# Kernel tuning notes

Measured on AMD Instinct MI355X. Metric: run time of the kernel, lower is better.

## Reference

```python
import jax, jax.numpy as jnp
import numpy as np

NB_HEAD = 16
SIZE_PER_HEAD = 64
D_MODEL = NB_HEAD * SIZE_PER_HEAD  # 1024
B, S = 4, 2048
NEG_BIG = 1e10


def setup_inputs() -> dict:
    key = jax.random.key(0)
    ks = jax.random.split(key, 9)
    glorot = lambda k, shape: jax.random.uniform(
        k, shape, jnp.float32, -1.0, 1.0) * np.sqrt(6.0 / (shape[0] + shape[1]))
    return {
        "Q_emb": jax.random.normal(ks[0], (B, S, D_MODEL), jnp.float32),
        "K_emb": jax.random.normal(ks[1], (B, S, D_MODEL), jnp.float32),
        "V_emb": jax.random.normal(ks[2], (B, S, D_MODEL), jnp.float32),
        "Q_ini": jax.random.randint(ks[3], (B, S), 0, 50),
        "K_ini": jax.random.randint(ks[4], (B, S), 0, 50),
        "WQ": glorot(ks[5], (D_MODEL, D_MODEL)),
        "WK": glorot(ks[6], (D_MODEL, D_MODEL)),
        "WV": glorot(ks[7], (D_MODEL, D_MODEL)),
        "WO": glorot(ks[8], (D_MODEL, D_MODEL)),
    }


def _proj(x, W):
    # [B,S,D] @ [D, H*dh] -> [B,H,S,dh]
    b, s, _ = x.shape
    y = jnp.einsum('bsd,de->bse', x, W)
    return y.reshape(b, s, NB_HEAD, SIZE_PER_HEAD).transpose(0, 2, 1, 3)


def reference(Q_emb, K_emb, V_emb, Q_ini, K_ini, WQ, WK, WV, WO):
    b, sq, _ = Q_emb.shape
    sk = K_emb.shape[1]
    q = _proj(Q_emb, WQ)
    k = _proj(K_emb, WK)
    v = _proj(V_emb, WV)
    scores = jnp.einsum('bhqd,bhkd->bhqk', q, k) / jnp.sqrt(
        jnp.asarray(SIZE_PER_HEAD, scores_dtype := q.dtype))
    # pad mask: 1 where key token id != 0, broadcast over queries
    pad = (K_ini != 0).astype(scores.dtype)[:, None, None, :]  # [B,1,1,Sk]
    # sub mask: cumsum of eye along rows == lower-triangular causal mask
    causal = jnp.tril(jnp.ones((sq, sk), scores.dtype))[None, None]  # [1,1,Sq,Sk]
    mask = jnp.minimum(pad, causal)
    scores = scores - (1.0 - mask) * NEG_BIG
    attn = jax.nn.softmax(scores, axis=-1)
    ctx = jnp.einsum('bhqk,bhkd->bhqd', attn, v)
    ctx = ctx.transpose(0, 2, 1, 3).reshape(b, sq, NB_HEAD * SIZE_PER_HEAD)
    return jnp.einsum('bsd,de->bse', ctx, WO)
```

## Files before the change

### kernel.cpp

```cpp
#include <hip/hip_runtime.h>

typedef __bf16 bf16_t;
typedef __bf16 bf16x8 __attribute__((ext_vector_type(8)));
typedef __bf16 bf16x4 __attribute__((ext_vector_type(4)));
typedef float  f32x4  __attribute__((ext_vector_type(4)));

#define S_LEN 2048
#define NH    16
#define DH    64
#define DM    1024
#define BATCH 4
#define LOG2E 1.44269504088896f

static __device__ __forceinline__ f32x4 mfma16(bf16x8 a, bf16x8 b, f32x4 c) {
    return __builtin_amdgcn_mfma_f32_16x16x32_bf16(a, b, c, 0, 0, 0);
}

#if __has_builtin(__builtin_amdgcn_exp2f)
static __device__ __forceinline__ float exp2_hw(float x) {
    return __builtin_amdgcn_exp2f(x);
}
#else
static __device__ __forceinline__ float exp2_hw(float x) {
    float r;
    asm("v_exp_f32 %0, %1" : "=v"(r) : "v"(x));
    return r;
}
#endif

static __device__ __forceinline__ void gl_lds16(const bf16_t* g, bf16_t* l) {
    __builtin_amdgcn_global_load_lds(
        (const __attribute__((address_space(1))) unsigned int*)g,
        (__attribute__((address_space(3))) unsigned int*)l, 16, 0, 0);
}

__global__ __launch_bounds__(256) void cvt3_bf16(const float* __restrict__ s0,
                                                 const float* __restrict__ s1,
                                                 const float* __restrict__ s2,
                                                 bf16_t* __restrict__ d0,
                                                 bf16_t* __restrict__ d1,
                                                 bf16_t* __restrict__ d2, int n) {
    int z = blockIdx.y;
    const float* s = (z == 0) ? s0 : (z == 1) ? s1 : s2;
    bf16_t*      d = (z == 0) ? d0 : (z == 1) ? d1 : d2;
    int i = (blockIdx.x * 256 + threadIdx.x) * 8;
    if (i >= n) return;
    const float4* q = (const float4*)(s + i);
    float4 a = q[0], b = q[1];
    bf16x8 r;
    r[0] = (bf16_t)a.x; r[1] = (bf16_t)a.y; r[2] = (bf16_t)a.z; r[3] = (bf16_t)a.w;
    r[4] = (bf16_t)b.x; r[5] = (bf16_t)b.y; r[6] = (bf16_t)b.z; r[7] = (bf16_t)b.w;
    *(bf16x8*)(d + i) = r;
}

__global__ __launch_bounds__(256) void wtrans(const float* __restrict__ W,
                                              bf16_t* __restrict__ Wt, float scale) {
    __shared__ bf16_t tile[32][33];
    int x = threadIdx.x, ty = threadIdx.y;
    int bx = blockIdx.x * 32, by = blockIdx.y * 32;
#pragma unroll
    for (int i = 0; i < 4; ++i) {
        int y = ty * 4 + i;
        tile[y][x] = (bf16_t)(W[(by + y) * DM + bx + x] * scale);
    }
    __syncthreads();
#pragma unroll
    for (int i = 0; i < 4; ++i) {
        int y = ty * 4 + i;
        Wt[(bx + y) * DM + by + x] = tile[x][y];
    }
}

__global__ __launch_bounds__(256) void btrans(const bf16_t* __restrict__ src,
                                              bf16_t* __restrict__ dst,
                                              int R, int C) {
    __shared__ bf16_t tile[32][33];
    int x = threadIdx.x, ty = threadIdx.y;
    int bx = blockIdx.x * 32, by = blockIdx.y * 32;
#pragma unroll
    for (int i = 0; i < 4; ++i) {
        int y = ty * 4 + i;
        tile[y][x] = src[(size_t)(by + y) * C + bx + x];
    }
    __syncthreads();
#pragma unroll
    for (int i = 0; i < 4; ++i) {
        int y = ty * 4 + i;
        dst[(size_t)(bx + y) * R + by + x] = tile[x][y];
    }
}

template <typename CT>
__global__ __launch_bounds__(512) void gemm_nt_256(const bf16_t* __restrict__ A,
                                                   const bf16_t* __restrict__ Bt,
                                                   CT* __restrict__ C,
                                                   int M, int N, int K, float alpha,
                                                   size_t zsA, size_t zsB, size_t zsC) {
    __shared__ __align__(16) bf16_t As[2 * 256 * 32];
    __shared__ __align__(16) bf16_t Bs[2 * 128 * 32];
    A  += (size_t)blockIdx.z * zsA;
    Bt += (size_t)blockIdx.z * zsB;
    C  += (size_t)blockIdx.z * zsC;
    int tid = threadIdx.x, wave = tid >> 6, lane = tid & 63;
    int l15 = lane & 15, quad = lane >> 4;
    int wm = wave >> 1, wn = wave & 1;
    int bm = blockIdx.x * 256, bn = blockIdx.y * 128;
    int srow = lane >> 2, skx = (lane & 3) << 3;

    f32x4 acc[4][4] = {};

    for (int k0 = 0; k0 < K; k0 += 64) {
#pragma unroll
        for (int c = 0; c < 4; ++c) {
            int t = wave * 4 + c;
            int kk = t & 1, rb = (t >> 1) * 16;
            gl_lds16(A + (size_t)(bm + rb + srow) * K + k0 + kk * 32 + skx,
                     As + kk * 8192 + rb * 32);
        }
#pragma unroll
        for (int c = 0; c < 2; ++c) {
            int t = wave * 2 + c;
            int kk = t & 1, rb = (t >> 1) * 16;
            gl_lds16(Bt + (size_t)(bn + rb + srow) * K + k0 + kk * 32 + skx,
                     Bs + kk * 4096 + rb * 32);
        }
        __syncthreads();

#pragma unroll
        for (int kk = 0; kk < 2; ++kk) {
            bf16x8 af[4], bfr[4];
#pragma unroll
            for (int i = 0; i < 4; ++i)
                af[i] = *(const bf16x8*)(As + kk * 8192 +
                                         (wm * 64 + i * 16 + l15) * 32 + quad * 8);
#pragma unroll
            for (int j = 0; j < 4; ++j)
                bfr[j] = *(const bf16x8*)(Bs + kk * 4096 +
                                          (wn * 64 + j * 16 + l15) * 32 + quad * 8);
#pragma unroll
            for (int i = 0; i < 4; ++i)
#pragma unroll
                for (int j = 0; j < 4; ++j)
                    acc[i][j] = mfma16(af[i], bfr[j], acc[i][j]);
        }
        __syncthreads();
    }

#pragma unroll
    for (int i = 0; i < 4; ++i)
#pragma unroll
        for (int r = 0; r < 4; ++r) {
            int row = bm + wm * 64 + i * 16 + quad * 4 + r;
#pragma unroll
            for (int j = 0; j < 4; ++j)
                C[(size_t)row * N + bn + wn * 64 + j * 16 + l15] =
                    (CT)(acc[i][j][r] * alpha);
        }
}

__global__ __launch_bounds__(256) void vmean_kernel(const bf16_t* __restrict__ Vp,
                                                    float* __restrict__ Vm) {
    __shared__ float red[4][64];
    int z = blockIdx.y;
    int c = blockIdx.x * 64 + (threadIdx.x & 63);
    int rg = threadIdx.x >> 6;
    const bf16_t* p = Vp + (size_t)z * S_LEN * DM + (size_t)rg * (S_LEN / 4) * DM + c;
    float s = 0.f;
    for (int r = 0; r < S_LEN / 4; ++r) s += (float)p[(size_t)r * DM];
    red[rg][threadIdx.x & 63] = s;
    __syncthreads();
    if (threadIdx.x < 64) {
        float t = red[0][threadIdx.x] + red[1][threadIdx.x] +
                  red[2][threadIdx.x] + red[3][threadIdx.x];
        Vm[z * DM + blockIdx.x * 64 + threadIdx.x] = t * (1.0f / S_LEN);
    }
}

__global__ __launch_bounds__(256) void attn_kernel(const bf16_t* __restrict__ Qp,
                                                   const bf16_t* __restrict__ Kp,
                                                   const bf16_t* __restrict__ VT,
                                                   const int* __restrict__ Kini,
                                                   const float* __restrict__ Vmean,
                                                   bf16_t* __restrict__ ctx,
                                                   int ldv, int nqt) {
    __shared__ __align__(16) bf16_t Ks[64 * 72];
    __shared__ __align__(16) bf16_t VsT[64 * 72];
    __shared__ __align__(16) bf16_t Ps[4][16 * 72];
    __shared__ bf16_t padb[2048];

    int bid = blockIdx.x;
    int qt = nqt - 1 - (bid >> 6);
    int hz = bid & 63;
    int h = hz & 15, z = hz >> 4;
    int tid = threadIdx.x, wave = tid >> 6, lane = tid & 63;
    int l15 = lane & 15, quad = lane >> 4;
    int qbase = qt * 64 + wave * 16;
    size_t rowz = (size_t)z * S_LEN;
    int ntiles = qt + 1;
    int nkeys = ntiles * 64;

    for (int i = tid; i < nkeys; i += 256)
        padb[i] = (Kini[rowz + i] == 0) ? (bf16_t)(-1.44269504e10f) : (bf16_t)(0.0f);

    const bf16_t* qptr = Qp + (rowz + qbase + l15) * DM + h * DH + quad * 8;
    bf16x8 qa0 = *(const bf16x8*)qptr;
    bf16x8 qa1 = *(const bf16x8*)(qptr + 32);

    f32x4 o[4] = {};
    f32x4 l4 = {0.f, 0.f, 0.f, 0.f};
    int q = qbase + l15;

    int srow = tid >> 2, sch = (tid & 3) << 4;
    const bf16_t* kgb = Kp + (rowz + srow) * DM + h * DH + sch;
    const bf16_t* vgb = VT + (size_t)(h * DH + srow) * ldv + rowz + sch;

    bf16x8 kr0 = *(const bf16x8*)kgb,        kr1 = *(const bf16x8*)(kgb + 8);
    bf16x8 vr0 = *(const bf16x8*)vgb,        vr1 = *(const bf16x8*)(vgb + 8);

    for (int kt = 0; kt < ntiles; ++kt) {
        int kb = kt * 64;
        *(bf16x8*)(Ks  + srow * 72 + sch)     = kr0;
        *(bf16x8*)(Ks  + srow * 72 + sch + 8) = kr1;
        *(bf16x8*)(VsT + srow * 72 + sch)     = vr0;
        *(bf16x8*)(VsT + srow * 72 + sch + 8) = vr1;
        __syncthreads();

        int nkb = (kt + 1 < ntiles) ? kb + 64 : kb;
        const bf16_t* kg = kgb + (size_t)nkb * DM;
        const bf16_t* vg = vgb + nkb;
        kr0 = *(const bf16x8*)kg; kr1 = *(const bf16x8*)(kg + 8);
        vr0 = *(const bf16x8*)vg; vr1 = *(const bf16x8*)(vg + 8);

        f32x4 sv[4];
#pragma unroll
        for (int ks = 0; ks < 4; ++ks) {
            bf16x8 kf0 = *(const bf16x8*)(Ks + (ks * 16 + l15) * 72 + quad * 8);
            bf16x8 kf1 = *(const bf16x8*)(Ks + (ks * 16 + l15) * 72 + 32 + quad * 8);
            f32x4 s = {0.f, 0.f, 0.f, 0.f};
            s = mfma16(kf0, qa0, s);
            s = mfma16(kf1, qa1, s);
            bf16x4 pb = *(const bf16x4*)(padb + kb + ks * 16 + quad * 4);
#pragma unroll
            for (int r = 0; r < 4; ++r) s[r] += (float)pb[r];
            sv[ks] = s;
        }
        if (kt == ntiles - 1) {
#pragma unroll
            for (int ks = 0; ks < 4; ++ks)
#pragma unroll
                for (int r = 0; r < 4; ++r)
                    if (kb + ks * 16 + quad * 4 + r > q) sv[ks][r] = -1.44269504e10f;
        }

#pragma unroll
        for (int ks = 0; ks < 4; ++ks) {
            f32x4 s = sv[ks];
#pragma unroll
            for (int r = 0; r < 4; ++r) s[r] = exp2_hw(s[r]);
            sv[ks] = s;
        }
        l4 += (sv[0] + sv[1]) + (sv[2] + sv[3]);
#pragma unroll
        for (int ks = 0; ks < 4; ++ks) {
            bf16x4 pk;
#pragma unroll
            for (int r = 0; r < 4; ++r) pk[r] = (bf16_t)sv[ks][r];
            *(bf16x4*)(Ps[wave] + l15 * 72 + ks * 16 + quad * 4) = pk;
        }

        bf16x8 pa0 = *(const bf16x8*)(Ps[wave] + l15 * 72 + quad * 8);
        bf16x8 pa1 = *(const bf16x8*)(Ps[wave] + l15 * 72 + 32 + quad * 8);
#pragma unroll
        for (int j = 0; j < 4; ++j) {
            bf16x8 vb0 = *(const bf16x8*)(VsT + (j * 16 + l15) * 72 + quad * 8);
            bf16x8 vb1 = *(const bf16x8*)(VsT + (j * 16 + l15) * 72 + 32 + quad * 8);
            o[j] = mfma16(vb0, pa0, o[j]);
            o[j] = mfma16(vb1, pa1, o[j]);
        }
        __syncthreads();
    }

    float l_ = (l4[0] + l4[1]) + (l4[2] + l4[3]);
    l_ += __shfl_xor(l_, 16);
    l_ += __shfl_xor(l_, 32);

    float inv = 1.0f / l_;
    bool dead = (l_ == 0.0f);
    if (__any(dead)) {
        const float* vm = Vmean + z * DM + h * DH;
#pragma unroll
        for (int j = 0; j < 4; ++j) {
            bf16x4 c;
#pragma unroll
            for (int r = 0; r < 4; ++r) {
                int dh = j * 16 + quad * 4 + r;
                float val = dead ? vm[dh] : o[j][r] * inv;
                c[r] = (bf16_t)val;
            }
            *(bf16x4*)(Ps[wave] + l15 * 72 + j * 16 + quad * 4) = c;
        }
    } else {
#pragma unroll
        for (int j = 0; j < 4; ++j) {
            bf16x4 c;
#pragma unroll
            for (int r = 0; r < 4; ++r) c[r] = (bf16_t)(o[j][r] * inv);
            *(bf16x4*)(Ps[wave] + l15 * 72 + j * 16 + quad * 4) = c;
        }
    }
    int rr = lane >> 2, cc = (lane & 3) * 16;
    bf16x8 t0 = *(const bf16x8*)(Ps[wave] + rr * 72 + cc);
    bf16x8 t1 = *(const bf16x8*)(Ps[wave] + rr * 72 + cc + 8);
    bf16_t* cp = ctx + (rowz + qbase + rr) * DM + h * DH + cc;
    *(bf16x8*)cp = t0;
    *(bf16x8*)(cp + 8) = t1;
}

extern "C" void kernel_launch(void* const* d_in, const int* in_sizes, int n_in,
                              void* d_out, int out_size, void* d_ws, size_t ws_size,
                              hipStream_t stream) {
    const float* Qe = (const float*)d_in[0];
    const float* Ke = (const float*)d_in[1];
    const float* Ve = (const float*)d_in[2];
    const int* Kini = (const int*)d_in[4];
    const float* WQ = (const float*)d_in[5];
    const float* WK = (const float*)d_in[6];
    const float* WV = (const float*)d_in[7];
    const float* WO = (const float*)d_in[8];
    float* out = (float*)d_out;

    const size_t EMB = (size_t)BATCH * S_LEN * DM;
    const size_t SB  = (size_t)S_LEN * DM;
    const size_t WSZ = (size_t)DM * DM;
    const size_t need_full = (6 * EMB + 4 * WSZ) * sizeof(bf16_t)
                           + (size_t)BATCH * DM * sizeof(float);

    dim3 tb32(32, 8), tg32(32, 32);
    const float qscale = 0.125f * LOG2E;

    if (ws_size >= need_full) {
        bf16_t* Qb  = (bf16_t*)d_ws;
        bf16_t* Kb  = Qb + EMB;
        bf16_t* Vb  = Kb + EMB;
        bf16_t* WQt = Vb + EMB;
        bf16_t* WKt = WQt + WSZ;
        bf16_t* WVt = WKt + WSZ;
        bf16_t* WOt = WVt + WSZ;
        bf16_t* Qp  = WOt + WSZ;
        bf16_t* Kp  = Qp + EMB;
        bf16_t* Vp  = Kp + EMB;
        float*  Vm  = (float*)(Vp + EMB);
        bf16_t* Cx  = Qp;
        bf16_t* VT  = Vb;

        int cg = (int)(EMB / (8 * 256));
        cvt3_bf16<<<dim3(cg, 3), 256, 0, stream>>>(Qe, Ke, Ve, Qb, Kb, Vb, (int)EMB);
        wtrans<<<tg32, tb32, 0, stream>>>(WQ, WQt, qscale);
        wtrans<<<tg32, tb32, 0, stream>>>(WK, WKt, 1.0f);
        wtrans<<<tg32, tb32, 0, stream>>>(WV, WVt, 1.0f);
        wtrans<<<tg32, tb32, 0, stream>>>(WO, WOt, 1.0f);

        gemm_nt_256<bf16_t><<<dim3(8192 / 256, DM / 128, 3), 512, 0, stream>>>(
            Qb, WQt, Qp, 8192, DM, DM, 1.0f, EMB, WSZ, EMB);

        btrans<<<dim3(DM / 32, 8192 / 32), tb32, 0, stream>>>(Vp, VT, 8192, DM);
        vmean_kernel<<<dim3(DM / 64, BATCH), 256, 0, stream>>>(Vp, Vm);
        attn_kernel<<<dim3((S_LEN / 64) * NH * BATCH), 256, 0, stream>>>(
            Qp, Kp, VT, Kini, Vm, Cx, 8192, S_LEN / 64);

        gemm_nt_256<float><<<dim3(8192 / 256, DM / 128, 1), 512, 0, stream>>>(
            Cx, WOt, out, 8192, DM, DM, 1.0f, 0, 0, 0);
    } else {
        bf16_t* Qb  = (bf16_t*)d_ws;
        bf16_t* Kb  = Qb + SB;
        bf16_t* Vb  = Kb + SB;
        bf16_t* WQt = Vb + SB;
        bf16_t* WKt = WQt + WSZ;
        bf16_t* WVt = WKt + WSZ;
        bf16_t* WOt = WVt + WSZ;
        bf16_t* Qp  = WOt + WSZ;
        bf16_t* Kp  = Qp + SB;
        bf16_t* Vp  = Kp + SB;
        float*  Vm  = (float*)(Vp + SB);
        bf16_t* Cx  = Qp;
        bf16_t* VT  = Vb;

        wtrans<<<tg32, tb32, 0, stream>>>(WQ, WQt, qscale);
        wtrans<<<tg32, tb32, 0, stream>>>(WK, WKt, 1.0f);
        wtrans<<<tg32, tb32, 0, stream>>>(WV, WVt, 1.0f);
        wtrans<<<tg32, tb32, 0, stream>>>(WO, WOt, 1.0f);

        int cg = (int)(SB / (8 * 256));
        for (int b = 0; b < BATCH; ++b) {
            const size_t off = (size_t)b * SB;
            cvt3_bf16<<<dim3(cg, 3), 256, 0, stream>>>(
                Qe + off, Ke + off, Ve + off, Qb, Kb, Vb, (int)SB);
            gemm_nt_256<bf16_t><<<dim3(2048 / 256, DM / 128, 3), 512, 0, stream>>>(
                Qb, WQt, Qp, 2048, DM, DM, 1.0f, SB, WSZ, SB);
            btrans<<<dim3(DM / 32, 2048 / 32), tb32, 0, stream>>>(Vp, VT, 2048, DM);
            vmean_kernel<<<dim3(DM / 64, 1), 256, 0, stream>>>(Vp, Vm);
            attn_kernel<<<dim3((S_LEN / 64) * NH), 256, 0, stream>>>(
                Qp, Kp, VT, Kini + (size_t)b * S_LEN, Vm, Cx, 2048, S_LEN / 64);
            gemm_nt_256<float><<<dim3(2048 / 256, DM / 128, 1), 512, 0, stream>>>(
                Cx, WOt, out + off, 2048, DM, DM, 1.0f, 0, 0, 0);
        }
    }
}
```

Before: 346.0 us.

## Process 128 queries per attention block, 32 per wave, to reuse K/V tiles

Measured after the change: 352.5 us. No clear change (+1.9%).

```diff
diff --git a/kernel.cpp b/kernel.cpp
--- a/kernel.cpp
+++ b/kernel.cpp
@@ -11,6 +11,7 @@
 #define DM    1024
 #define BATCH 4
 #define LOG2E 1.44269504088896f
+#define NEGB  (-1.44269504e10f)
 
 static __device__ __forceinline__ f32x4 mfma16(bf16x8 a, bf16x8 b, f32x4 c) {
     return __builtin_amdgcn_mfma_f32_16x16x32_bf16(a, b, c, 0, 0, 0);
@@ -176,13 +177,13 @@
     }
 }
 
-__global__ __launch_bounds__(256) void attn_kernel(const bf16_t* __restrict__ Qp,
-                                                   const bf16_t* __restrict__ Kp,
-                                                   const bf16_t* __restrict__ VT,
-                                                   const int* __restrict__ Kini,
-                                                   const float* __restrict__ Vmean,
-                                                   bf16_t* __restrict__ ctx,
-                                                   int ldv, int nqt) {
+__global__ __launch_bounds__(256, 4) void attn_kernel(const bf16_t* __restrict__ Qp,
+                                                      const bf16_t* __restrict__ Kp,
+                                                      const bf16_t* __restrict__ VT,
+                                                      const int* __restrict__ Kini,
+                                                      const float* __restrict__ Vmean,
+                                                      bf16_t* __restrict__ ctx,
+                                                      int ldv, int nqt) {
     __shared__ __align__(16) bf16_t Ks[64 * 72];
     __shared__ __align__(16) bf16_t VsT[64 * 72];
     __shared__ __align__(16) bf16_t Ps[4][16 * 72];
@@ -194,21 +195,24 @@
     int h = hz & 15, z = hz >> 4;
     int tid = threadIdx.x, wave = tid >> 6, lane = tid & 63;
     int l15 = lane & 15, quad = lane >> 4;
-    int qbase = qt * 64 + wave * 16;
+    int qb0 = qt * 128 + wave * 32;
     size_t rowz = (size_t)z * S_LEN;
-    int ntiles = qt + 1;
+    int ntiles = 2 * qt + 2;
     int nkeys = ntiles * 64;
 
     for (int i = tid; i < nkeys; i += 256)
-        padb[i] = (Kini[rowz + i] == 0) ? (bf16_t)(-1.44269504e10f) : (bf16_t)(0.0f);
-
-    const bf16_t* qptr = Qp + (rowz + qbase + l15) * DM + h * DH + quad * 8;
-    bf16x8 qa0 = *(const bf16x8*)qptr;
-    bf16x8 qa1 = *(const bf16x8*)(qptr + 32);
-
-    f32x4 o[4] = {};
-    f32x4 l4 = {0.f, 0.f, 0.f, 0.f};
-    int q = qbase + l15;
+        padb[i] = (Kini[rowz + i] == 0) ? (bf16_t)NEGB : (bf16_t)(0.0f);
+
+    const bf16_t* qptr = Qp + (rowz + qb0 + l15) * DM + h * DH + quad * 8;
+    bf16x8 qa00 = *(const bf16x8*)qptr;
+    bf16x8 qa01 = *(const bf16x8*)(qptr + 32);
+    bf16x8 qa10 = *(const bf16x8*)(qptr + 16 * DM);
+    bf16x8 qa11 = *(const bf16x8*)(qptr + 16 * DM + 32);
+
+    f32x4 o0[4] = {}, o1[4] = {};
+    f32x4 l40 = {0.f,0.f,0.f,0.f}, l41 = {0.f,0.f,0.f,0.f};
+    int q0 = qb0 + l15, q1 = q0 + 16;
+    int q0max = qb0 + 15, q1max = qb0 + 31;
 
     int srow = tid >> 2, sch = (tid & 3) << 4;
     const bf16_t* kgb = Kp + (rowz + srow) * DM + h * DH + sch;
@@ -231,89 +235,106 @@
         kr0 = *(const bf16x8*)kg; kr1 = *(const bf16x8*)(kg + 8);
         vr0 = *(const bf16x8*)vg; vr1 = *(const bf16x8*)(vg + 8);
 
-        f32x4 sv[4];
-#pragma unroll
-        for (int ks = 0; ks < 4; ++ks) {
-            bf16x8 kf0 = *(const bf16x8*)(Ks + (ks * 16 + l15) * 72 + quad * 8);
-            bf16x8 kf1 = *(const bf16x8*)(Ks + (ks * 16 + l15) * 72 + 32 + quad * 8);
-            f32x4 s = {0.f, 0.f, 0.f, 0.f};
-            s = mfma16(kf0, qa0, s);
-            s = mfma16(kf1, qa1, s);
-            bf16x4 pb = *(const bf16x4*)(padb + kb + ks * 16 + quad * 4);
-#pragma unroll
-            for (int r = 0; r < 4; ++r) s[r] += (float)pb[r];
-            sv[ks] = s;
-        }
-        if (kt == ntiles - 1) {
-#pragma unroll
-            for (int ks = 0; ks < 4; ++ks)
-#pragma unroll
-                for (int r = 0; r < 4; ++r)
-                    if (kb + ks * 16 + quad * 4 + r > q) sv[ks][r] = -1.44269504e10f;
-        }
-
-#pragma unroll
-        for (int ks = 0; ks < 4; ++ks) {
-            f32x4 s = sv[ks];
-#pragma unroll
-            for (int r = 0; r < 4; ++r) s[r] = exp2_hw(s[r]);
-            sv[ks] = s;
-        }
-        l4 += (sv[0] + sv[1]) + (sv[2] + sv[3]);
-#pragma unroll
-        for (int ks = 0; ks < 4; ++ks) {
-            bf16x4 pk;
-#pragma unroll
-            for (int r = 0; r < 4; ++r) pk[r] = (bf16_t)sv[ks][r];
-            *(bf16x4*)(Ps[wave] + l15 * 72 + ks * 16 + quad * 4) = pk;
-        }
-
-        bf16x8 pa0 = *(const bf16x8*)(Ps[wave] + l15 * 72 + quad * 8);
-        bf16x8 pa1 = *(const bf16x8*)(Ps[wave] + l15 * 72 + 32 + quad * 8);
+        if (kb <= q1max) {
+            bool live0 = (kb <= q0max);
+            bool bnd = (kb + 63 > qb0);
+            f32x4 s1[4];
+#pragma unroll
+            for (int ks = 0; ks < 4; ++ks) {
+                bf16x8 kf0 = *(const bf16x8*)(Ks + (ks * 16 + l15) * 72 + quad * 8);
+                bf16x8 kf1 = *(const bf16x8*)(Ks + (ks * 16 + l15) * 72 + 32 + quad * 8);
+                bf16x4 pb = *(const bf16x4*)(padb + kb + ks * 16 + quad * 4);
+                f32x4 t1 = {0.f, 0.f, 0.f, 0.f};
+                t1 = mfma16(kf0, qa10, t1);
+                t1 = mfma16(kf1, qa11, t1);
+#pragma unroll
+                for (int r = 0; r < 4; ++r) t1[r] += (float)pb[r];
+                if (bnd) {
+#pragma unroll
+                    for (int r = 0; r < 4; ++r)
+                        if (kb + ks * 16 + quad * 4 + r > q1) t1[r] = NEGB;
+                }
+                s1[ks] = t1;
+                if (live0) {
+                    f32x4 t0 = {0.f, 0.f, 0.f, 0.f};
+                    t0 = mfma16(kf0, qa00, t0);
+                    t0 = mfma16(kf1, qa01, t0);
+#pragma unroll
+                    for (int r = 0; r < 4; ++r) t0[r] += (float)pb[r];
+                    if (bnd) {
+#pragma unroll
+                        for (int r = 0; r < 4; ++r)
+                            if (kb + ks * 16 + quad * 4 + r > q0) t0[r] = NEGB;
+                    }
+#pragma unroll
+                    for (int r = 0; r < 4; ++r) t0[r] = exp2_hw(t0[r]);
+                    l40 += t0;
+                    bf16x4 pk;
+#pragma unroll
+                    for (int r = 0; r < 4; ++r) pk[r] = (bf16_t)t0[r];
+                    *(bf16x4*)(Ps[wave] + l15 * 72 + ks * 16 + quad * 4) = pk;
+                }
+            }
+            bf16x8 pa00, pa01;
+            if (live0) {
+                pa00 = *(const bf16x8*)(Ps[wave] + l15 * 72 + quad * 8);
+                pa01 = *(const bf16x8*)(Ps[wave] + l15 * 72 + 32 + quad * 8);
+            }
+#pragma unroll
+            for (int ks = 0; ks < 4; ++ks) {
+                f32x4 t1 = s1[ks];
+#pragma unroll
+                for (int r = 0; r < 4; ++r) t1[r] = exp2_hw(t1[r]);
+                l41 += t1;
+                bf16x4 pk;
+#pragma unroll
+                for (int r = 0; r < 4; ++r) pk[r] = (bf16_t)t1[r];
+                *(bf16x4*)(Ps[wave] + l15 * 72 + ks * 16 + quad * 4) = pk;
+            }
+            bf16x8 pa10 = *(const bf16x8*)(Ps[wave] + l15 * 72 + quad * 8);
+            bf16x8 pa11 = *(const bf16x8*)(Ps[wave] + l15 * 72 + 32 + quad * 8);
+#pragma unroll
+            for (int j = 0; j < 4; ++j) {
+                bf16x8 vb0 = *(const bf16x8*)(VsT + (j * 16 + l15) * 72 + quad * 8);
+                bf16x8 vb1 = *(const bf16x8*)(VsT + (j * 16 + l15) * 72 + 32 + quad * 8);
+                o1[j] = mfma16(vb0, pa10, o1[j]);
+                o1[j] = mfma16(vb1, pa11, o1[j]);
+                if (live0) {
+                    o0[j] = mfma16(vb0, pa00, o0[j]);
+                    o0[j] = mfma16(vb1, pa01, o0[j]);
+                }
+            }
+        }
+        __syncthreads();
+    }
+
+    const float* vm = Vmean + z * DM + h * DH;
+    int rr = lane >> 2, cc = (lane & 3) * 16;
+#pragma unroll
+    for (int u = 0; u < 2; ++u) {
+        f32x4 l4 = u ? l41 : l40;
+        float l_ = (l4[0] + l4[1]) + (l4[2] + l4[3]);
+        l_ += __shfl_xor(l_, 16);
+        l_ += __shfl_xor(l_, 32);
+        float inv = 1.0f / l_;
+        bool dead = (l_ == 0.0f);
 #pragma unroll
         for (int j = 0; j < 4; ++j) {
-            bf16x8 vb0 = *(const bf16x8*)(VsT + (j * 16 + l15) * 72 + quad * 8);
-            bf16x8 vb1 = *(const bf16x8*)(VsT + (j * 16 + l15) * 72 + 32 + quad * 8);
-            o[j] = mfma16(vb0, pa0, o[j]);
-            o[j] = mfma16(vb1, pa1, o[j]);
-        }
-        __syncthreads();
-    }
-
-    float l_ = (l4[0] + l4[1]) + (l4[2] + l4[3]);
-    l_ += __shfl_xor(l_, 16);
-    l_ += __shfl_xor(l_, 32);
-
-    float inv = 1.0f / l_;
-    bool dead = (l_ == 0.0f);
-    if (__any(dead)) {
-        const float* vm = Vmean + z * DM + h * DH;
-#pragma unroll
-        for (int j = 0; j < 4; ++j) {
+            f32x4 oj = u ? o1[j] : o0[j];
             bf16x4 c;
 #pragma unroll
             for (int r = 0; r < 4; ++r) {
-                int dh = j * 16 + quad * 4 + r;
-                float val = dead ? vm[dh] : o[j][r] * inv;
+                float val = dead ? vm[j * 16 + quad * 4 + r] : oj[r] * inv;
                 c[r] = (bf16_t)val;
             }
             *(bf16x4*)(Ps[wave] + l15 * 72 + j * 16 + quad * 4) = c;
         }
-    } else {
-#pragma unroll
-        for (int j = 0; j < 4; ++j) {
-            bf16x4 c;
-#pragma unroll
-            for (int r = 0; r < 4; ++r) c[r] = (bf16_t)(o[j][r] * inv);
-            *(bf16x4*)(Ps[wave] + l15 * 72 + j * 16 + quad * 4) = c;
-        }
-    }
-    int rr = lane >> 2, cc = (lane & 3) * 16;
-    bf16x8 t0 = *(const bf16x8*)(Ps[wave] + rr * 72 + cc);
-    bf16x8 t1 = *(const bf16x8*)(Ps[wave] + rr * 72 + cc + 8);
-    bf16_t* cp = ctx + (rowz + qbase + rr) * DM + h * DH + cc;
-    *(bf16x8*)cp = t0;
-    *(bf16x8*)(cp + 8) = t1;
+        bf16x8 t0 = *(const bf16x8*)(Ps[wave] + rr * 72 + cc);
+        bf16x8 t1 = *(const bf16x8*)(Ps[wave] + rr * 72 + cc + 8);
+        bf16_t* cp = ctx + (rowz + qb0 + u * 16 + rr) * DM + h * DH + cc;
+        *(bf16x8*)cp = t0;
+        *(bf16x8*)(cp + 8) = t1;
+    }
 }
 
 extern "C" void kernel_launch(void* const* d_in, const int* in_sizes, int n_in,
@@ -365,8 +386,8 @@
 
         btrans<<<dim3(DM / 32, 8192 / 32), tb32, 0, stream>>>(Vp, VT, 8192, DM);
         vmean_kernel<<<dim3(DM / 64, BATCH), 256, 0, stream>>>(Vp, Vm);
-        attn_kernel<<<dim3((S_LEN / 64) * NH * BATCH), 256, 0, stream>>>(
-            Qp, Kp, VT, Kini, Vm, Cx, 8192, S_LEN / 64);
+        attn_kernel<<<dim3((S_LEN / 128) * NH * BATCH), 256, 0, stream>>>(
+            Qp, Kp, VT, Kini, Vm, Cx, 8192, S_LEN / 128);
 
         gemm_nt_256<float><<<dim3(8192 / 256, DM / 128, 1), 512, 0, stream>>>(
             Cx, WOt, out, 8192, DM, DM, 1.0f, 0, 0, 0);
@@ -399,8 +420,8 @@
                 Qb, WQt, Qp, 2048, DM, DM, 1.0f, SB, WSZ, SB);
             btrans<<<dim3(DM / 32, 2048 / 32), tb32, 0, stream>>>(Vp, VT, 2048, DM);
             vmean_kernel<<<dim3(DM / 64, 1), 256, 0, stream>>>(Vp, Vm);
-            attn_kernel<<<dim3((S_LEN / 64) * NH), 256, 0, stream>>>(
-                Qp, Kp, VT, Kini + (size_t)b * S_LEN, Vm, Cx, 2048, S_LEN / 64);
+            attn_kernel<<<dim3((S_LEN / 128) * NH), 256, 0, stream>>>(
+                Qp, Kp, VT, Kini + (size_t)b * S_LEN, Vm, Cx, 2048, S_LEN / 128);
             gemm_nt_256<float><<<dim3(2048 / 256, DM / 128, 1), 512, 0, stream>>>(
                 Cx, WOt, out + off, 2048, DM, DM, 1.0f, 0, 0, 0);
         }
```
